# Kernel tuning notes

Measured on AMD Instinct MI355X. Metric: run time of the kernel, lower is better.

Reference implementation:

```python
import jax, jax.numpy as jnp
import numpy as np

LEVEL_SHAPES = np.array([[16, 40, 40], [8, 20, 20], [4, 10, 10]], dtype=np.int32)


def _trilinear_sample(vol, grid):
    """Replicates F.grid_sample(mode='bilinear', padding_mode='zeros', align_corners=False).
    vol:  (B, C, T, H, W)
    grid: (B, Q, 3) with last dim (x, y, z) -> indexes (W, H, T), values in [-1, 1]
    returns (B, Q, C)
    """
    B, C, T, H, W = vol.shape
    gx, gy, gz = grid[..., 0], grid[..., 1], grid[..., 2]
    # unnormalize (align_corners=False)
    x = ((gx + 1.0) * W - 1.0) * 0.5
    y = ((gy + 1.0) * H - 1.0) * 0.5
    z = ((gz + 1.0) * T - 1.0) * 0.5
    x0 = jnp.floor(x); y0 = jnp.floor(y); z0 = jnp.floor(z)
    fx = x - x0; fy = y - y0; fz = z - z0
    x0i = x0.astype(jnp.int32); y0i = y0.astype(jnp.int32); z0i = z0.astype(jnp.int32)
    vol_flat = vol.reshape(B, C, T * H * W).transpose(0, 2, 1)  # (B, THW, C)
    out = jnp.zeros(grid.shape[:2] + (C,), dtype=vol.dtype)
    for dz in (0, 1):
        wz = fz if dz else (1.0 - fz)
        zi = z0i + dz
        for dy in (0, 1):
            wy = fy if dy else (1.0 - fy)
            yi = y0i + dy
            for dx in (0, 1):
                wx = fx if dx else (1.0 - fx)
                xi = x0i + dx
                valid = ((xi >= 0) & (xi < W) & (yi >= 0) & (yi < H) & (zi >= 0) & (zi < T))
                idx = jnp.clip((zi * H + yi) * W + xi, 0, T * H * W - 1)
                g = jnp.take_along_axis(vol_flat, idx[..., None], axis=1)  # (B, Q, C)
                out = out + g * (wx * wy * wz * valid.astype(vol.dtype))[..., None]
    return out


def reference(value, value_spatial_shapes, sampling_locations, attention_weights):
    """ms_deform_attn_core_pytorch_3D in jax.
    value: (N, S, M, D); sampling_locations: (N, Lq, M, L, P, 3) in [0,1];
    attention_weights: (N, Lq, M, L, P); returns (N, Lq, M*D)."""
    shapes = np.asarray(value_spatial_shapes)  # static level shapes
    N, S, M, D = value.shape
    _, Lq, _, L, P, _ = sampling_locations.shape
    grids = 2.0 * sampling_locations - 1.0  # (N, Lq, M, L, P, 3)
    sizes = [int(t * h * w) for t, h, w in shapes]
    offs = np.concatenate([[0], np.cumsum(sizes)])
    sampled = []
    for l in range(L):
        T_, H_, W_ = (int(v) for v in shapes[l])
        # (N, THW, M, D) -> (N*M, D, T, H, W)
        v = value[:, offs[l]:offs[l + 1]].transpose(0, 2, 3, 1).reshape(N * M, D, T_, H_, W_)
        # (N, Lq, M, P, 3) -> (N*M, Lq*P, 3)
        g = grids[:, :, :, l].transpose(0, 2, 1, 3, 4).reshape(N * M, Lq * P, 3)
        s = _trilinear_sample(v, g).reshape(N * M, Lq, P, D)
        sampled.append(s)
    sampled = jnp.stack(sampled, axis=2).reshape(N * M, Lq, L * P, D)
    aw = attention_weights.transpose(0, 2, 1, 3, 4).reshape(N * M, Lq, L * P)
    out = jnp.einsum('bqk,bqkd->bqd', aw, sampled)  # (N*M, Lq, D)
    return out.reshape(N, M, Lq, D).transpose(0, 2, 1, 3).reshape(N, Lq, M * D)


def setup_inputs() -> dict:
    key = jax.random.key(0)
    k1, k2, k3 = jax.random.split(key, 3)
    N, M, D = 2, 8, 32
    L, P = 3, 4
    S = int(np.prod(LEVEL_SHAPES, axis=1).sum())  # 29200
    Lq = S
    value = jax.random.normal(k1, (N, S, M, D), dtype=jnp.float32)
    sampling_locations = jax.random.uniform(k2, (N, Lq, M, L, P, 3), dtype=jnp.float32)
    aw = jax.random.normal(k3, (N, Lq, M, L, P), dtype=jnp.float32)
    aw = jax.nn.softmax(aw.reshape(N, Lq, M, L * P), axis=-1).reshape(N, Lq, M, L, P)
    return {
        'value': value,
        'value_spatial_shapes': np.asarray(LEVEL_SHAPES),
        'sampling_locations': sampling_locations,
        'attention_weights': aw,
    }
```

## Files before the change

### kernel.cpp

```cpp
#include <hip/hip_runtime.h>
#include <hip/hip_bf16.h>

typedef float    f32x4 __attribute__((ext_vector_type(4)));
typedef unsigned u32x4 __attribute__((ext_vector_type(4)));

constexpr int kN  = 2;
constexpr int kS  = 29200;
constexpr int kM  = 8;
constexpr int kD  = 32;
constexpr int kL  = 3;
constexpr int kP  = 4;
constexpr int kLq = 29200;

constexpr int kGroups  = 32;
constexpr int kQChunks = (kLq + kGroups - 1) / kGroups;
constexpr int kBlocks  = kN * kM * kQChunks;

constexpr size_t kWsData = (size_t)kN * kS * kM * kD * 2;
constexpr size_t kWsNeed = kWsData + 128;

constexpr int kSlotV = 3;
constexpr int kGrpV  = 12 * kSlotV + 1;
constexpr int kLdsV  = kGroups * kGrpV;

__device__ __forceinline__ f32x4 ntload4(const float* p) {
  return __builtin_nontemporal_load(reinterpret_cast<const f32x4*>(p));
}

__global__ __launch_bounds__(256) void cvtT_kernel(
    const float* __restrict__ in, unsigned short* __restrict__ outb)
{
  const int g     = blockIdx.x * 256 + threadIdx.x;
  const int lane4 = g & 3;
  const int site  = g >> 2;
  const int s  = site % kS;
  const int nm = site / kS;
  const int m  = nm & 7;
  const int n  = nm >> 3;
  const float* ip = in + ((size_t)(n * kS + s) * kM + m) * kD + lane4 * 8;
  const f32x4 a = ntload4(ip);
  const f32x4 b = ntload4(ip + 4);
  unsigned short r[8];
  r[0] = __bfloat16_as_ushort(__float2bfloat16(a[0]));
  r[1] = __bfloat16_as_ushort(__float2bfloat16(a[1]));
  r[2] = __bfloat16_as_ushort(__float2bfloat16(a[2]));
  r[3] = __bfloat16_as_ushort(__float2bfloat16(a[3]));
  r[4] = __bfloat16_as_ushort(__float2bfloat16(b[0]));
  r[5] = __bfloat16_as_ushort(__float2bfloat16(b[1]));
  r[6] = __bfloat16_as_ushort(__float2bfloat16(b[2]));
  r[7] = __bfloat16_as_ushort(__float2bfloat16(b[3]));
  u32x4 pk;
  pk[0] = (unsigned)r[0] | ((unsigned)r[1] << 16);
  pk[1] = (unsigned)r[2] | ((unsigned)r[3] << 16);
  pk[2] = (unsigned)r[4] | ((unsigned)r[5] << 16);
  pk[3] = (unsigned)r[6] | ((unsigned)r[7] << 16);
  *reinterpret_cast<u32x4*>(outb + (size_t)site * kD + lane4 * 8) = pk;
}

__global__ __launch_bounds__(256, 6) void msda3d_bf16_kernel(
    const char* __restrict__ wsbase,
    const float* __restrict__ sloc,
    const float* __restrict__ attw,
    float* __restrict__ out)
{
  __shared__ u32x4 lds_v[kLdsV];

  const int bid    = blockIdx.x;
  const int xcd    = bid & 7;
  const int li     = bid >> 3;
  const int half   = (li >= kQChunks) ? 1 : 0;
  const int combo  = xcd * 2 + half;
  const int qblock = li - half * kQChunks;
  const int n = combo >> 3;
  const int m = combo & 7;
  const int tid = threadIdx.x;

  for (int pidx = tid; pidx < 384; pidx += 256) {
    const int pt = pidx >> 5;
    const int g  = pidx & 31;
    const int l  = pt >> 2;
    const int T  = 16 >> l;
    const int H  = 40 >> l;
    const int W  = 40 >> l;
    const int base = (l == 0) ? 0 : ((l == 1) ? 25600 : 28800);

    int q = qblock * kGroups + g;
    if (q >= kLq) q = kLq - 1;
    const size_t qm = (size_t)(n * kLq + q) * kM + m;
    const float gx = sloc[qm * 36 + pt * 3 + 0];
    const float gy = sloc[qm * 36 + pt * 3 + 1];
    const float gz = sloc[qm * 36 + pt * 3 + 2];
    const float aw = attw[qm * 12 + pt];

    const float x = gx * (float)W - 0.5f;
    const float y = gy * (float)H - 0.5f;
    const float z = gz * (float)T - 0.5f;
    const float xf = floorf(x), yf = floorf(y), zf = floorf(z);
    const float fx = x - xf, fy = y - yf, fz = z - zf;
    const int x0 = (int)xf, y0 = (int)yf, z0 = (int)zf;
    const int x1 = x0 + 1, y1 = y0 + 1, z1 = z0 + 1;
    const bool vx0 = (unsigned)x0 < (unsigned)W;
    const bool vx1 = (unsigned)x1 < (unsigned)W;
    const bool vy0 = (unsigned)y0 < (unsigned)H;
    const bool vy1 = (unsigned)y1 < (unsigned)H;
    const bool vz0 = (unsigned)z0 < (unsigned)T;
    const bool vz1 = (unsigned)z1 < (unsigned)T;
    const int yc0 = vy0 ? y0 : 0, yc1 = vy1 ? y1 : 0;
    const int zc0 = vz0 ? z0 : 0, zc1 = vz1 ? z1 : 0;
    const int r00 = (zc0 * H + yc0) * W;
    const int r01 = (zc0 * H + yc1) * W;
    const int r10 = (zc1 * H + yc0) * W;
    const int r11 = (zc1 * H + yc1) * W;
    const float wx0 = (1.f - fx) * aw, wx1 = fx * aw;
    const float wy0 = 1.f - fy, wy1 = fy;
    const float wz0 = 1.f - fz, wz1 = fz;
    const float w00 = wz0 * wy0, w01 = wz0 * wy1;
    const float w10 = wz1 * wy0, w11 = wz1 * wy1;
    const bool o00 = vz0 && vy0, o01 = vz0 && vy1;
    const bool o10 = vz1 && vy0, o11 = vz1 && vy1;

    u32x4 offs, wA, wB;
    offs[0] = (unsigned)(base + r00 + x0 + 1) << 6;
    offs[1] = (unsigned)(base + r01 + x0 + 1) << 6;
    offs[2] = (unsigned)(base + r10 + x0 + 1) << 6;
    offs[3] = (unsigned)(base + r11 + x0 + 1) << 6;
    wA[0] = __float_as_uint((o00 && vx0) ? w00 * wx0 : 0.f);
    wA[1] = __float_as_uint((o01 && vx0) ? w01 * wx0 : 0.f);
    wA[2] = __float_as_uint((o10 && vx0) ? w10 * wx0 : 0.f);
    wA[3] = __float_as_uint((o11 && vx0) ? w11 * wx0 : 0.f);
    wB[0] = __float_as_uint((o00 && vx1) ? w00 * wx1 : 0.f);
    wB[1] = __float_as_uint((o01 && vx1) ? w01 * wx1 : 0.f);
    wB[2] = __float_as_uint((o10 && vx1) ? w10 * wx1 : 0.f);
    wB[3] = __float_as_uint((o11 && vx1) ? w11 * wx1 : 0.f);

    u32x4* slot = lds_v + g * kGrpV + pt * kSlotV;
    slot[0] = offs;
    slot[1] = wA;
    slot[2] = wB;
  }
  __syncthreads();

  const int group = tid >> 3;
  const int lane8 = tid & 7;
  const int q = qblock * kGroups + group;

  const char* __restrict__ vbase =
      wsbase + (size_t)combo * (kS * kD * 2);
  const unsigned loff = (unsigned)lane8 * 16u;
  const bool hiLane = (lane8 >= 4);
  const u32x4* slot0 = lds_v + group * kGrpV;

  f32x4 acc0 = {0.f, 0.f, 0.f, 0.f};
  f32x4 acc1 = {0.f, 0.f, 0.f, 0.f};

#pragma unroll 1
  for (int pt = 0; pt < 12; ++pt) {
    const u32x4 offs = slot0[pt * kSlotV + 0];
    const u32x4 wA   = slot0[pt * kSlotV + 1];
    const u32x4 wB   = slot0[pt * kSlotV + 2];

#pragma unroll
    for (int i = 0; i < 4; ++i) {
      const float w_ = __uint_as_float(hiLane ? wB[i] : wA[i]);
      const u32x4 v = *reinterpret_cast<const u32x4*>(vbase + offs[i] + loff);
      acc0[0] = fmaf(__uint_as_float(v[0] << 16),         w_, acc0[0]);
      acc0[1] = fmaf(__uint_as_float(v[0] & 0xffff0000u), w_, acc0[1]);
      acc0[2] = fmaf(__uint_as_float(v[1] << 16),         w_, acc0[2]);
      acc0[3] = fmaf(__uint_as_float(v[1] & 0xffff0000u), w_, acc0[3]);
      acc1[0] = fmaf(__uint_as_float(v[2] << 16),         w_, acc1[0]);
      acc1[1] = fmaf(__uint_as_float(v[2] & 0xffff0000u), w_, acc1[1]);
      acc1[2] = fmaf(__uint_as_float(v[3] << 16),         w_, acc1[2]);
      acc1[3] = fmaf(__uint_as_float(v[3] & 0xffff0000u), w_, acc1[3]);
    }
  }

  f32x4 s0, s1;
#pragma unroll
  for (int j = 0; j < 4; ++j) {
    s0[j] = acc0[j] + __shfl_xor(acc0[j], 4);
    s1[j] = acc1[j] + __shfl_xor(acc1[j], 4);
  }
  const f32x4 stv = hiLane ? s1 : s0;

  if (q < kLq) {
    float* __restrict__ op = out + (size_t)(n * kLq + q) * (kM * kD) + m * kD +
                             (lane8 & 3) * 8 + (lane8 >> 2) * 4;
    __builtin_nontemporal_store(stv, reinterpret_cast<f32x4*>(op));
  }
}

__device__ __forceinline__ f32x4 load16f(const float* base, unsigned byteoff) {
  return *reinterpret_cast<const f32x4*>(
      reinterpret_cast<const char*>(base) + byteoff);
}

__global__ __launch_bounds__(256) void msda3d_f32_kernel(
    const float* __restrict__ value,
    const float* __restrict__ sloc,
    const float* __restrict__ attw,
    float* __restrict__ out)
{
  constexpr int LT[3]   = {16, 8, 4};
  constexpr int LH[3]   = {40, 20, 10};
  constexpr int LW[3]   = {40, 20, 10};
  constexpr int LOFF[3] = {0, 25600, 28800};

  const int bid    = blockIdx.x;
  const int xcd    = bid & 7;
  const int li     = bid >> 3;
  const int half   = (li >= kQChunks) ? 1 : 0;
  const int combo  = xcd * 2 + half;
  const int qblock = li - half * kQChunks;
  const int n = combo >> 3;
  const int m = combo & 7;

  const int group = threadIdx.x >> 3;
  const int lane8 = threadIdx.x & 7;
  const int q = qblock * kGroups + group;
  if (q >= kLq) return;

  const size_t qm = (size_t)(n * kLq + q) * kM + m;
  const float* __restrict__ lp = sloc + qm * (kL * kP * 3);
  const float* __restrict__ wp = attw + qm * (kL * kP);
  const float* __restrict__ vbase = value + ((size_t)n * kS * kM + m) * kD;
  const unsigned loff = (unsigned)lane8 * 16u;

  f32x4 acc = {0.f, 0.f, 0.f, 0.f};

#pragma unroll
  for (int l = 0; l < kL; ++l) {
    const int T = LT[l], H = LH[l], W = LW[l];
    const unsigned ubase = ((unsigned)LOFF[l] << 10) + loff;

    const f32x4 c0 = ntload4(lp + l * 12 + 0);
    const f32x4 c1 = ntload4(lp + l * 12 + 4);
    const f32x4 c2 = ntload4(lp + l * 12 + 8);
    const f32x4 w4 = ntload4(wp + l * 4);
    const float crd[12] = {c0[0], c0[1], c0[2], c0[3],
                           c1[0], c1[1], c1[2], c1[3],
                           c2[0], c2[1], c2[2], c2[3]};
    const float aww[4] = {w4[0], w4[1], w4[2], w4[3]};

#pragma unroll
    for (int p = 0; p < kP; ++p) {
      const float gx = crd[p * 3 + 0];
      const float gy = crd[p * 3 + 1];
      const float gz = crd[p * 3 + 2];
      const float aw = aww[p];
      const float x = gx * (float)W - 0.5f;
      const float y = gy * (float)H - 0.5f;
      const float z = gz * (float)T - 0.5f;
      const float xf = floorf(x), yf = floorf(y), zf = floorf(z);
      const float fx = x - xf, fy = y - yf, fz = z - zf;
      const int x0 = (int)xf, y0 = (int)yf, z0 = (int)zf;
      const int x1 = x0 + 1, y1 = y0 + 1, z1 = z0 + 1;
      const bool vx0 = (unsigned)x0 < (unsigned)W;
      const bool vx1 = (unsigned)x1 < (unsigned)W;
      const bool vy0 = (unsigned)y0 < (unsigned)H;
      const bool vy1 = (unsigned)y1 < (unsigned)H;
      const bool vz0 = (unsigned)z0 < (unsigned)T;
      const bool vz1 = (unsigned)z1 < (unsigned)T;
      const int xc0 = vx0 ? x0 : 0, xc1 = vx1 ? x1 : 0;
      const int yc0 = vy0 ? y0 : 0, yc1 = vy1 ? y1 : 0;
      const int zc0 = vz0 ? z0 : 0, zc1 = vz1 ? z1 : 0;
      const int r00 = (zc0 * H + yc0) * W;
      const int r01 = (zc0 * H + yc1) * W;
      const int r10 = (zc1 * H + yc0) * W;
      const int r11 = (zc1 * H + yc1) * W;
      const float wx0 = (1.f - fx) * aw, wx1 = fx * aw;
      const float wy0 = 1.f - fy, wy1 = fy;
      const float wz0 = 1.f - fz, wz1 = fz;
      const float w00 = wz0 * wy0, w01 = wz0 * wy1;
      const float w10 = wz1 * wy0, w11 = wz1 * wy1;
      const bool o00 = vz0 && vy0, o01 = vz0 && vy1;
      const bool o10 = vz1 && vy0, o11 = vz1 && vy1;

      unsigned off[8];
      float cw[8];
      off[0] = ubase + ((unsigned)(r00 + xc0) << 10);
      off[1] = ubase + ((unsigned)(r00 + xc1) << 10);
      off[2] = ubase + ((unsigned)(r01 + xc0) << 10);
      off[3] = ubase + ((unsigned)(r01 + xc1) << 10);
      off[4] = ubase + ((unsigned)(r10 + xc0) << 10);
      off[5] = ubase + ((unsigned)(r10 + xc1) << 10);
      off[6] = ubase + ((unsigned)(r11 + xc0) << 10);
      off[7] = ubase + ((unsigned)(r11 + xc1) << 10);
      cw[0] = (o00 && vx0) ? w00 * wx0 : 0.f;
      cw[1] = (o00 && vx1) ? w00 * wx1 : 0.f;
      cw[2] = (o01 && vx0) ? w01 * wx0 : 0.f;
      cw[3] = (o01 && vx1) ? w01 * wx1 : 0.f;
      cw[4] = (o10 && vx0) ? w10 * wx0 : 0.f;
      cw[5] = (o10 && vx1) ? w10 * wx1 : 0.f;
      cw[6] = (o11 && vx0) ? w11 * wx0 : 0.f;
      cw[7] = (o11 && vx1) ? w11 * wx1 : 0.f;

      f32x4 v[8];
#pragma unroll
      for (int c = 0; c < 8; ++c) v[c] = load16f(vbase, off[c]);
#pragma unroll
      for (int c = 0; c < 8; ++c) acc += v[c] * cw[c];
    }
  }

  float* __restrict__ op =
      out + (size_t)(n * kLq + q) * (kM * kD) + m * kD + lane8 * 4;
  __builtin_nontemporal_store(acc, reinterpret_cast<f32x4*>(op));
}

extern "C" void kernel_launch(void* const* d_in, const int* in_sizes, int n_in,
                              void* d_out, int out_size, void* d_ws, size_t ws_size,
                              hipStream_t stream) {
  const float* value = (const float*)d_in[0];
  const float* sloc  = (const float*)d_in[2];
  const float* attw  = (const float*)d_in[3];
  float* out = (float*)d_out;

  if (ws_size >= kWsNeed) {
    unsigned short* valb = (unsigned short*)((char*)d_ws + 64);
    const int nThreads = kN * kM * kS * 4;
    cvtT_kernel<<<nThreads / 256, 256, 0, stream>>>(value, valb);
    msda3d_bf16_kernel<<<kBlocks, 256, 0, stream>>>(
        (const char*)d_ws, sloc, attw, out);
  } else {
    msda3d_f32_kernel<<<kBlocks, 256, 0, stream>>>(value, sloc, attw, out);
  }
}
```

Before: 164.7 us.

## Duplicate bf16 value buffer and route odd sites to the shifted copy

The conversion kernel now writes the bf16 value tensor twice: once at the workspace base and once at an offset of data size plus 64 bytes. The sampling kernel sends odd-indexed sites to the shifted copy, so each 64-byte site row lands in a differently aligned cache-line position depending on parity. The likely aim is to change how neighbouring corner gathers map onto 128-byte lines or channels. The cost is twice the conversion write traffic and double the workspace footprint, and the path is taken only when the workspace is large enough.

```diff
diff --git a/kernel.cpp b/kernel.cpp
--- a/kernel.cpp
+++ b/kernel.cpp
@@ -16,8 +16,11 @@
 constexpr int kQChunks = (kLq + kGroups - 1) / kGroups;
 constexpr int kBlocks  = kN * kM * kQChunks;
 
-constexpr size_t kWsData = (size_t)kN * kS * kM * kD * 2;
-constexpr size_t kWsNeed = kWsData + 128;
+constexpr size_t kData      = (size_t)kN * kS * kM * kD * 2;
+constexpr size_t kCopyOff   = kData + 64;
+constexpr size_t kWsNeedDup = 2 * kData + 320;
+constexpr size_t kWsNeed1   = kData + 128;
+constexpr int    kSliceB    = kS * kD * 2;
 
 constexpr int kSlotV = 3;
 constexpr int kGrpV  = 12 * kSlotV + 1;
@@ -28,7 +31,8 @@
 }
 
 __global__ __launch_bounds__(256) void cvtT_kernel(
-    const float* __restrict__ in, unsigned short* __restrict__ outb)
+    const float* __restrict__ in, char* __restrict__ outb,
+    unsigned long long copyOff)
 {
   const int g     = blockIdx.x * 256 + threadIdx.x;
   const int lane4 = g & 3;
@@ -54,11 +58,14 @@
   pk[1] = (unsigned)r[2] | ((unsigned)r[3] << 16);
   pk[2] = (unsigned)r[4] | ((unsigned)r[5] << 16);
   pk[3] = (unsigned)r[6] | ((unsigned)r[7] << 16);
-  *reinterpret_cast<u32x4*>(outb + (size_t)site * kD + lane4 * 8) = pk;
-}
-
+  char* p0 = outb + (size_t)site * 64 + lane4 * 16;
+  *reinterpret_cast<u32x4*>(p0) = pk;
+  if (copyOff) *reinterpret_cast<u32x4*>(p0 + copyOff) = pk;
+}
+
+template <int DUP>
 __global__ __launch_bounds__(256, 6) void msda3d_bf16_kernel(
-    const char* __restrict__ wsbase,
+    const char* __restrict__ db,
     const float* __restrict__ sloc,
     const float* __restrict__ attw,
     float* __restrict__ out)
@@ -119,11 +126,23 @@
     const bool o00 = vz0 && vy0, o01 = vz0 && vy1;
     const bool o10 = vz1 && vy0, o11 = vz1 && vy1;
 
+    const int s0 = base + r00 + x0;
+    const int s1 = base + r01 + x0;
+    const int s2 = base + r10 + x0;
+    const int s3 = base + r11 + x0;
+
     u32x4 offs, wA, wB;
-    offs[0] = (unsigned)(base + r00 + x0 + 1) << 6;
-    offs[1] = (unsigned)(base + r01 + x0 + 1) << 6;
-    offs[2] = (unsigned)(base + r10 + x0 + 1) << 6;
-    offs[3] = (unsigned)(base + r11 + x0 + 1) << 6;
+    if (DUP) {
+      offs[0] = (unsigned)((s0 & 1) ? (size_t)kCopyOff + s0 * 64 : s0 * 64);
+      offs[1] = (unsigned)((s1 & 1) ? (size_t)kCopyOff + s1 * 64 : s1 * 64);
+      offs[2] = (unsigned)((s2 & 1) ? (size_t)kCopyOff + s2 * 64 : s2 * 64);
+      offs[3] = (unsigned)((s3 & 1) ? (size_t)kCopyOff + s3 * 64 : s3 * 64);
+    } else {
+      offs[0] = (unsigned)(s0 + 1) << 6;
+      offs[1] = (unsigned)(s1 + 1) << 6;
+      offs[2] = (unsigned)(s2 + 1) << 6;
+      offs[3] = (unsigned)(s3 + 1) << 6;
+    }
     wA[0] = __float_as_uint((o00 && vx0) ? w00 * wx0 : 0.f);
     wA[1] = __float_as_uint((o01 && vx0) ? w01 * wx0 : 0.f);
     wA[2] = __float_as_uint((o10 && vx0) ? w10 * wx0 : 0.f);
@@ -144,8 +163,7 @@
   const int lane8 = tid & 7;
   const int q = qblock * kGroups + group;
 
-  const char* __restrict__ vbase =
-      wsbase + (size_t)combo * (kS * kD * 2);
+  const char* __restrict__ vbase = db + (size_t)combo * kSliceB;
   const unsigned loff = (unsigned)lane8 * 16u;
   const bool hiLane = (lane8 >= 4);
   const u32x4* slot0 = lds_v + group * kGrpV;
@@ -174,13 +192,13 @@
     }
   }
 
-  f32x4 s0, s1;
+  f32x4 s0v, s1v;
 #pragma unroll
   for (int j = 0; j < 4; ++j) {
-    s0[j] = acc0[j] + __shfl_xor(acc0[j], 4);
-    s1[j] = acc1[j] + __shfl_xor(acc1[j], 4);
-  }
-  const f32x4 stv = hiLane ? s1 : s0;
+    s0v[j] = acc0[j] + __shfl_xor(acc0[j], 4);
+    s1v[j] = acc1[j] + __shfl_xor(acc1[j], 4);
+  }
+  const f32x4 stv = hiLane ? s1v : s0v;
 
   if (q < kLq) {
     float* __restrict__ op = out + (size_t)(n * kLq + q) * (kM * kD) + m * kD +
@@ -315,11 +333,15 @@
   const float* attw  = (const float*)d_in[3];
   float* out = (float*)d_out;
 
-  if (ws_size >= kWsNeed) {
-    unsigned short* valb = (unsigned short*)((char*)d_ws + 64);
-    const int nThreads = kN * kM * kS * 4;
-    cvtT_kernel<<<nThreads / 256, 256, 0, stream>>>(value, valb);
-    msda3d_bf16_kernel<<<kBlocks, 256, 0, stream>>>(
+  const int nThreads = kN * kM * kS * 4;
+  if (ws_size >= kWsNeedDup) {
+    char* e = (char*)d_ws + 128;
+    cvtT_kernel<<<nThreads / 256, 256, 0, stream>>>(value, e, kCopyOff);
+    msda3d_bf16_kernel<1><<<kBlocks, 256, 0, stream>>>(e, sloc, attw, out);
+  } else if (ws_size >= kWsNeed1) {
+    char* e = (char*)d_ws + 64;
+    cvtT_kernel<<<nThreads / 256, 256, 0, stream>>>(value, e, 0ull);
+    msda3d_bf16_kernel<0><<<kBlocks, 256, 0, stream>>>(
         (const char*)d_ws, sloc, attw, out);
   } else {
     msda3d_f32_kernel<<<kBlocks, 256, 0, stream>>>(value, sloc, attw, out);
```

Result: no change. 164.8 us (+0.0%).
